# Optimization experiments

Measured on AMD Instinct MI355X. Metric: run time of the kernel, lower is better.

## Reference

```python
import jax, jax.numpy as jnp
import numpy as np

B, L, D = 2, 2048, 2048
NH, HD = 16, 128
SCALE = HD ** -0.5


def setup_inputs() -> dict:
    key = jax.random.key(0)
    ks = jax.random.split(key, 9)
    s = D ** -0.5  # roughly torch Linear init scale
    return {
        "hidden_states": jax.random.normal(ks[0], (B, L, D), dtype=jnp.float32),
        "Wq": jax.random.normal(ks[1], (NH * HD, D), dtype=jnp.float32) * s,
        "bq": jnp.zeros((NH * HD,), dtype=jnp.float32),
        "Wk": jax.random.normal(ks[2], (NH * HD, D), dtype=jnp.float32) * s,
        "bk": jnp.zeros((NH * HD,), dtype=jnp.float32),
        "Wv": jax.random.normal(ks[3], (NH * HD, D), dtype=jnp.float32) * s,
        "bv": jnp.zeros((NH * HD,), dtype=jnp.float32),
        "Wo": jax.random.normal(ks[4], (D, NH * HD), dtype=jnp.float32) * s,
        "bo": jnp.zeros((D,), dtype=jnp.float32),
    }


def reference(hidden_states, Wq, bq, Wk, bk, Wv, bv, Wo, bo):
    # projections (torch Linear: x @ W.T + b), split into heads: b s h d
    q = (hidden_states @ Wq.T + bq).reshape(B, L, NH, HD)
    k = (hidden_states @ Wk.T + bk).reshape(B, L, NH, HD)
    v = (hidden_states @ Wv.T + bv).reshape(B, L, NH, HD)
    # scores: [B, NH, L, L]
    scores = jnp.einsum("bqhd,bkhd->bhqk", q, k) * SCALE
    causal = jnp.tril(jnp.ones((L, L), dtype=bool))  # True = keep
    scores = jnp.where(causal, scores, jnp.float32(-jnp.inf))
    probs = jax.nn.softmax(scores, axis=-1)
    out = jnp.einsum("bhqk,bkhd->bqhd", probs, v).reshape(B, L, NH * HD)
    return out @ Wo.T + bo
```

## Files before the change

### kernel.cpp

```cpp
#include <hip/hip_runtime.h>

#define B_  2
#define L_  2048
#define D_  2048
#define NH_ 16
#define HD_ 128

typedef __bf16 bf16_t;
typedef __bf16 bf16x8 __attribute__((ext_vector_type(8)));
typedef __bf16 bf16x4 __attribute__((ext_vector_type(4)));
typedef float  f32x4  __attribute__((ext_vector_type(4)));

typedef const __attribute__((address_space(1))) void* gas_ptr;
typedef __attribute__((address_space(3))) void* las_ptr;

__device__ __forceinline__ void g2l16(const void* g, void* l) {
    __builtin_amdgcn_global_load_lds((gas_ptr)g, (las_ptr)l, 16, 0, 0);
}

__device__ __forceinline__ void raw_barrier() {
    asm volatile("s_barrier" ::: "memory");
}
__device__ __forceinline__ void wait_vm8() {
    asm volatile("s_waitcnt vmcnt(8)" ::: "memory");
}
__device__ __forceinline__ void wait_vm4() {
    asm volatile("s_waitcnt vmcnt(4)" ::: "memory");
}
__device__ __forceinline__ void wait_vm0() {
    asm volatile("s_waitcnt vmcnt(0)" ::: "memory");
}

__global__ __launch_bounds__(256) void cvt_all(const float* __restrict__ X,
                                               const float* __restrict__ Wq,
                                               const float* __restrict__ Wk,
                                               const float* __restrict__ Wv,
                                               const float* __restrict__ Wo,
                                               bf16_t* __restrict__ Xb,
                                               bf16_t* __restrict__ Wqkvb,
                                               bf16_t* __restrict__ Wob) {
    int i = blockIdx.x * 256 + threadIdx.x;
    const float* src;
    bf16_t* dst;
    int off;
    if (i < 2097152) { src = X; dst = Xb; off = i; }
    else {
        int j = i - 2097152;
        int w = j >> 20;
        off = j & 1048575;
        src = (w == 0) ? Wq : (w == 1) ? Wk : (w == 2) ? Wv : Wo;
        dst = (w == 3) ? Wob : Wqkvb + (size_t)w * 4194304;
    }
    float4 v = ((const float4*)src)[off];
    bf16x4 o;
    o[0] = (bf16_t)v.x; o[1] = (bf16_t)v.y; o[2] = (bf16_t)v.z; o[3] = (bf16_t)v.w;
    ((bf16x4*)dst)[off] = o;
}

__global__ __launch_bounds__(256) void gemm_bt(const bf16_t* __restrict__ A,
                                               const bf16_t* __restrict__ Bw,
                                               const float* __restrict__ bias,
                                               float* __restrict__ C,
                                               int M, int N, int K) {
    constexpr int BK = 32;
    __shared__ __align__(16) bf16_t smem[16384];
    const int tid  = threadIdx.x;
    const int wave = tid >> 6, lane = tid & 63;
    const int quad = lane >> 4, l16 = lane & 15;
    const int tm = blockIdx.y * 128, tn = blockIdx.x * 128;
    const int wm = (wave >> 1) * 64, wn = (wave & 1) * 64;

    const int srow = wave * 16 + (lane >> 2);
    const int scol = (lane & 3) * 8;
    const bf16_t* Ag = A  + (size_t)(tm + srow) * K + scol;
    const bf16_t* Bg = Bw + (size_t)(tn + srow) * K + scol;
    const size_t rowskip = (size_t)64 * K;

    auto stage = [&](int k0, int p) {
        bf16_t* a = smem + p * 4096 + (wave * 16) * BK;
        bf16_t* bl = smem + 8192 + p * 4096 + (wave * 16) * BK;
        g2l16(Ag + k0, a);
        g2l16(Ag + k0 + rowskip, a + 64 * BK);
        g2l16(Bg + k0, bl);
        g2l16(Bg + k0 + rowskip, bl + 64 * BK);
    };

    f32x4 acc[4][4] = {};
    const int niter = K / BK;
    stage(0, 0);

    for (int i = 0; i < niter; ++i) {
        const int p = i & 1;
        if (i + 1 < niter) { stage((i + 1) * BK, p ^ 1); wait_vm4(); }
        else wait_vm0();
        raw_barrier();

        const bf16_t* Alp = smem + p * 4096;
        const bf16_t* Blp = smem + 8192 + p * 4096;
        bf16x8 af[4], bf[4];
#pragma unroll
        for (int ii = 0; ii < 4; ++ii)
            af[ii] = *(const bf16x8*)(Alp + (wm + ii * 16 + l16) * BK + quad * 8);
#pragma unroll
        for (int j = 0; j < 4; ++j)
            bf[j] = *(const bf16x8*)(Blp + (wn + j * 16 + l16) * BK + quad * 8);
#pragma unroll
        for (int ii = 0; ii < 4; ++ii)
#pragma unroll
            for (int j = 0; j < 4; ++j)
                acc[ii][j] = __builtin_amdgcn_mfma_f32_16x16x32_bf16(af[ii], bf[j], acc[ii][j], 0, 0, 0);
        raw_barrier();
    }

#pragma unroll
    for (int j = 0; j < 4; ++j) {
        const int col = tn + wn + j * 16 + l16;
        const float bv = bias[col];
#pragma unroll
        for (int i = 0; i < 4; ++i) {
            const int row0 = tm + wm + i * 16 + quad * 4;
#pragma unroll
            for (int r = 0; r < 4; ++r)
                C[(size_t)(row0 + r) * N + col] = acc[i][j][r] + bv;
        }
    }
}

__global__ __launch_bounds__(256) void gemm_qkv(const bf16_t* __restrict__ A,
                                                const bf16_t* __restrict__ Bw,
                                                const float* __restrict__ b0,
                                                const float* __restrict__ b1,
                                                const float* __restrict__ b2,
                                                bf16_t* __restrict__ QK,
                                                bf16_t* __restrict__ Vt) {
    constexpr int BK = 32, K = D_;
    __shared__ __align__(16) bf16_t smem[17408];
    const int tid  = threadIdx.x;
    const int wave = tid >> 6, lane = tid & 63;
    const int quad = lane >> 4, l16 = lane & 15;
    const int tm = blockIdx.y * 128, tn = blockIdx.x * 128;
    const int wm = (wave >> 1) * 64, wn = (wave & 1) * 64;

    const int seg = tn >> 11;
    const float* bias = (seg == 0) ? b0 : (seg == 1) ? b1 : b2;

    const int srow = wave * 16 + (lane >> 2);
    const int scol = (lane & 3) * 8;
    const bf16_t* Ag = A  + (size_t)(tm + srow) * K + scol;
    const bf16_t* Bg = Bw + (size_t)(tn + srow) * K + scol;
    const size_t rowskip = (size_t)64 * K;

    auto stage = [&](int k0, int p) {
        bf16_t* a = smem + p * 4096 + (wave * 16) * BK;
        bf16_t* bl = smem + 8192 + p * 4096 + (wave * 16) * BK;
        g2l16(Ag + k0, a);
        g2l16(Ag + k0 + rowskip, a + 64 * BK);
        g2l16(Bg + k0, bl);
        g2l16(Bg + k0 + rowskip, bl + 64 * BK);
    };

    f32x4 acc[4][4] = {};
    const int niter = K / BK;
    stage(0, 0);

    for (int i = 0; i < niter; ++i) {
        const int p = i & 1;
        if (i + 1 < niter) { stage((i + 1) * BK, p ^ 1); wait_vm4(); }
        else wait_vm0();
        raw_barrier();

        const bf16_t* Alp = smem + p * 4096;
        const bf16_t* Blp = smem + 8192 + p * 4096;
        bf16x8 af[4], bf[4];
#pragma unroll
        for (int ii = 0; ii < 4; ++ii)
            af[ii] = *(const bf16x8*)(Alp + (wm + ii * 16 + l16) * BK + quad * 8);
#pragma unroll
        for (int j = 0; j < 4; ++j)
            bf[j] = *(const bf16x8*)(Blp + (wn + j * 16 + l16) * BK + quad * 8);
#pragma unroll
        for (int ii = 0; ii < 4; ++ii)
#pragma unroll
            for (int j = 0; j < 4; ++j)
                acc[ii][j] = __builtin_amdgcn_mfma_f32_16x16x32_bf16(af[ii], bf[j], acc[ii][j], 0, 0, 0);
        raw_barrier();
    }

    if (seg < 2) {
#pragma unroll
        for (int j = 0; j < 4; ++j) {
            const int col = tn + wn + j * 16 + l16;
            const float bv = bias[col & 2047];
#pragma unroll
            for (int i = 0; i < 4; ++i) {
                const int row0 = tm + wm + i * 16 + quad * 4;
#pragma unroll
                for (int r = 0; r < 4; ++r)
                    QK[(size_t)(row0 + r) * 4096 + col] = (bf16_t)(acc[i][j][r] + bv);
            }
        }
    } else {
        const int h = (tn >> 7) - 32;
        const int b = tm >> 11;
        const int tokbase = tm & 2047;
        __syncthreads();
#pragma unroll
        for (int j = 0; j < 4; ++j) {
            const int d = wn + j * 16 + l16;
            const float bv = bias[(tn + wn + j * 16 + l16) & 2047];
#pragma unroll
            for (int i = 0; i < 4; ++i)
#pragma unroll
                for (int r = 0; r < 4; ++r) {
                    const int tok = wm + i * 16 + quad * 4 + r;
                    smem[d * 136 + (((tok >> 3) ^ (d & 7)) << 3) + (tok & 7)] =
                        (bf16_t)(acc[i][j][r] + bv);
                }
        }
        __syncthreads();
        const int d = tid >> 1, half = tid & 1;
        bf16_t* gp = Vt + ((size_t)(b * NH_ + h) * HD_ + d) * L_ + tokbase + half * 64;
#pragma unroll
        for (int c2 = 0; c2 < 8; ++c2) {
            const int cc = half * 8 + c2;
            bf16x8 v = *(const bf16x8*)(smem + d * 136 + ((cc ^ (d & 7)) << 3));
            *(bf16x8*)(gp + c2 * 8) = v;
        }
    }
}

__global__ __launch_bounds__(256, 2) void attn_kernel(const bf16_t* __restrict__ QK,
                                                      const bf16_t* __restrict__ Vt,
                                                      bf16_t* __restrict__ Ctx) {
    constexpr float SCALE = 0.08838834764831845f;
    constexpr float MFIX  = 8.0f;
    const int bid = blockIdx.x;
    const int bh = bid & 31;
    const int qt = 15 - (bid >> 5);
    const int b = bh >> 4, h = bh & 15;
    const int tid = threadIdx.x, wave = tid >> 6, lane = tid & 63;
    const int quad = lane >> 4, l16 = lane & 15;
    const int q0 = qt * 128;

    __shared__ bf16_t Kl[2][64 * 128];
    __shared__ bf16_t Vl[2][128 * 64];
    __shared__ bf16_t Pl[4][16 * 72];

    bf16x8 qf[2][4];
#pragma unroll
    for (int s = 0; s < 2; ++s) {
        const bf16_t* qp = QK + (size_t)(b * L_ + q0 + wave * 32 + s * 16 + l16) * 4096 + h * HD_ + quad * 8;
#pragma unroll
        for (int ks = 0; ks < 4; ++ks) qf[s][ks] = *(const bf16x8*)(qp + ks * 32);
    }

    bf16x8 ones;
#pragma unroll
    for (int j = 0; j < 8; ++j) ones[j] = (bf16_t)1.0f;

    f32x4 oacc[2][8] = {};
    f32x4 lacc[2] = {};

    const bf16_t* Kg = QK + (size_t)(b * L_) * 4096 + 2048 + h * HD_;
    const bf16_t* Vg = Vt + (size_t)(bh * HD_) * L_;

    auto stage = [&](int tile, int p) {
        const bf16_t* kg = Kg + (size_t)tile * 64 * 4096;
        const bf16_t* vg = Vg + tile * 64;
#pragma unroll
        for (int c = 0; c < 4; ++c) {
            int row = c * 16 + wave * 4 + (lane >> 4);
            int gcol = ((lane & 15) ^ (row & 15)) * 8;
            g2l16(kg + (size_t)row * 4096 + gcol, &Kl[p][(c * 16 + wave * 4) * 128]);
        }
#pragma unroll
        for (int c = 0; c < 4; ++c) {
            int row = c * 32 + wave * 8 + (lane >> 3);
            int gcol = ((lane & 7) ^ (row & 7)) * 8;
            g2l16(vg + (size_t)row * L_ + gcol, &Vl[p][(c * 32 + wave * 8) * 64]);
        }
    };

    const int n = 2 * qt + 2;
    stage(0, 0);

    for (int it = 0; it < n; ++it) {
        const int p = it & 1;
        if (it + 1 < n) {
            stage(it + 1, p ^ 1);
            wait_vm8();
        } else {
            wait_vm0();
        }
        raw_barrier();

        const int kb = it * 64;
        const bool need_mask = (it >= n - 2);

        f32x4 sa[2][4] = {};
#pragma unroll
        for (int nt = 0; nt < 4; ++nt) {
            const int krow = nt * 16 + l16;
#pragma unroll
            for (int ks = 0; ks < 4; ++ks) {
                bf16x8 kf = *(const bf16x8*)(&Kl[p][krow * 128 + (((ks * 4 + quad) ^ l16) * 8)]);
                sa[0][nt] = __builtin_amdgcn_mfma_f32_16x16x32_bf16(qf[0][ks], kf, sa[0][nt], 0, 0, 0);
                sa[1][nt] = __builtin_amdgcn_mfma_f32_16x16x32_bf16(qf[1][ks], kf, sa[1][nt], 0, 0, 0);
            }
        }

        bf16x8 pf0[2], pf1[2];
#pragma unroll
        for (int nt = 0; nt < 4; ++nt)
#pragma unroll
            for (int r = 0; r < 4; ++r) {
                float sv = sa[0][nt][r] * SCALE - MFIX;
                if (need_mask) {
                    const int key = kb + nt * 16 + l16;
                    const int qq = q0 + wave * 32 + quad * 4 + r;
                    sv = (key <= qq) ? sv : -1e30f;
                }
                Pl[wave][(quad * 4 + r) * 72 + nt * 16 + l16] = (bf16_t)__expf(sv);
            }
        pf0[0] = *(const bf16x8*)(&Pl[wave][l16 * 72 + quad * 8]);
        pf0[1] = *(const bf16x8*)(&Pl[wave][l16 * 72 + 32 + quad * 8]);

#pragma unroll
        for (int nt = 0; nt < 4; ++nt)
#pragma unroll
            for (int r = 0; r < 4; ++r) {
                float sv = sa[1][nt][r] * SCALE - MFIX;
                if (need_mask) {
                    const int key = kb + nt * 16 + l16;
                    const int qq = q0 + wave * 32 + 16 + quad * 4 + r;
                    sv = (key <= qq) ? sv : -1e30f;
                }
                Pl[wave][(quad * 4 + r) * 72 + nt * 16 + l16] = (bf16_t)__expf(sv);
            }
        pf1[0] = *(const bf16x8*)(&Pl[wave][l16 * 72 + quad * 8]);
        pf1[1] = *(const bf16x8*)(&Pl[wave][l16 * 72 + 32 + quad * 8]);

        lacc[0] = __builtin_amdgcn_mfma_f32_16x16x32_bf16(pf0[0], ones, lacc[0], 0, 0, 0);
        lacc[0] = __builtin_amdgcn_mfma_f32_16x16x32_bf16(pf0[1], ones, lacc[0], 0, 0, 0);
        lacc[1] = __builtin_amdgcn_mfma_f32_16x16x32_bf16(pf1[0], ones, lacc[1], 0, 0, 0);
        lacc[1] = __builtin_amdgcn_mfma_f32_16x16x32_bf16(pf1[1], ones, lacc[1], 0, 0, 0);

#pragma unroll
        for (int dt = 0; dt < 8; ++dt) {
            const int drow = dt * 16 + l16;
#pragma unroll
            for (int ks = 0; ks < 2; ++ks) {
                bf16x8 vf = *(const bf16x8*)(&Vl[p][drow * 64 + (((ks * 4 + quad) ^ (drow & 7)) * 8)]);
                oacc[0][dt] = __builtin_amdgcn_mfma_f32_16x16x32_bf16(pf0[ks], vf, oacc[0][dt], 0, 0, 0);
                oacc[1][dt] = __builtin_amdgcn_mfma_f32_16x16x32_bf16(pf1[ks], vf, oacc[1][dt], 0, 0, 0);
            }
        }
        raw_barrier();
    }

#pragma unroll
    for (int s = 0; s < 2; ++s)
#pragma unroll
        for (int r = 0; r < 4; ++r) {
            const float inv = 1.0f / lacc[s][r];
            const int q = q0 + wave * 32 + s * 16 + quad * 4 + r;
            bf16_t* cp = Ctx + (size_t)(b * L_ + q) * 2048 + h * HD_;
#pragma unroll
            for (int dt = 0; dt < 8; ++dt)
                cp[dt * 16 + l16] = (bf16_t)(oacc[s][dt][r] * inv);
        }
}

extern "C" void kernel_launch(void* const* d_in, const int* in_sizes, int n_in,
                              void* d_out, int out_size, void* d_ws, size_t ws_size,
                              hipStream_t stream) {
    const float* X  = (const float*)d_in[0];
    const float* Wq = (const float*)d_in[1];
    const float* bq = (const float*)d_in[2];
    const float* Wk = (const float*)d_in[3];
    const float* bk = (const float*)d_in[4];
    const float* Wv = (const float*)d_in[5];
    const float* bv = (const float*)d_in[6];
    const float* Wo = (const float*)d_in[7];
    const float* bo = (const float*)d_in[8];
    float* out = (float*)d_out;

    char* ws = (char*)d_ws;
    bf16_t* Xb   = (bf16_t*)(ws);
    bf16_t* Ctx  = (bf16_t*)(ws);
    bf16_t* Wqkv = (bf16_t*)(ws + 16777216);
    bf16_t* Wob  = (bf16_t*)(ws + 41943040);
    bf16_t* QKb  = (bf16_t*)(ws + 50331648);
    bf16_t* Vtb  = (bf16_t*)(ws + 83886080);

    cvt_all<<<24576, 256, 0, stream>>>(X, Wq, Wk, Wv, Wo, Xb, Wqkv, Wob);

    gemm_qkv<<<dim3(48, 32), 256, 0, stream>>>(Xb, Wqkv, bq, bk, bv, QKb, Vtb);

    attn_kernel<<<dim3(512), 256, 0, stream>>>(QKb, Vtb, Ctx);

    gemm_bt<<<dim3(16, 32), 256, 0, stream>>>(Ctx, Wob, bo, out,
                                              B_ * L_, D_, D_);
}
```

Before: 380.7 us.

## Rewrite QKV GEMM with 256x256 tiles, 8 waves, swizzled LDS and interleaved staging

Rewrites the fused QKV projection GEMM to use 256x256 output tiles with 512 threads, BK=64 and XOR-swizzled LDS layout. Global-to-LDS loads for the next K tile are split into quarters and interleaved between four MFMA sub-phases, with s_setprio raised around the MFMA bursts. The V transpose epilogue now goes through per-wave LDS regions. This aims to raise arithmetic intensity and cut LDS bank conflicts, at the cost of more registers, 128KB LDS per block and a grid of only 384 blocks.

```diff
diff --git a/kernel.cpp b/kernel.cpp
--- a/kernel.cpp
+++ b/kernel.cpp
@@ -26,6 +26,9 @@
 }
 __device__ __forceinline__ void wait_vm4() {
     asm volatile("s_waitcnt vmcnt(4)" ::: "memory");
+}
+__device__ __forceinline__ void wait_vm2() {
+    asm volatile("s_waitcnt vmcnt(2)" ::: "memory");
 }
 __device__ __forceinline__ void wait_vm0() {
     asm volatile("s_waitcnt vmcnt(0)" ::: "memory");
@@ -126,105 +129,185 @@
     }
 }
 
-__global__ __launch_bounds__(256) void gemm_qkv(const bf16_t* __restrict__ A,
-                                                const bf16_t* __restrict__ Bw,
-                                                const float* __restrict__ b0,
-                                                const float* __restrict__ b1,
-                                                const float* __restrict__ b2,
-                                                bf16_t* __restrict__ QK,
-                                                bf16_t* __restrict__ Vt) {
-    constexpr int BK = 32, K = D_;
-    __shared__ __align__(16) bf16_t smem[17408];
+__global__ __launch_bounds__(512, 2) void gemm_qkv(const bf16_t* __restrict__ A,
+                                                   const bf16_t* __restrict__ Bw,
+                                                   const float* __restrict__ b0,
+                                                   const float* __restrict__ b1,
+                                                   const float* __restrict__ b2,
+                                                   bf16_t* __restrict__ QK,
+                                                   bf16_t* __restrict__ Vt) {
+    constexpr int K  = D_;
+    constexpr int BK = 64;
+    constexpr int NT = K / BK;
+    __shared__ __align__(16) bf16_t smem[65536];
+
     const int tid  = threadIdx.x;
     const int wave = tid >> 6, lane = tid & 63;
     const int quad = lane >> 4, l16 = lane & 15;
-    const int tm = blockIdx.y * 128, tn = blockIdx.x * 128;
-    const int wm = (wave >> 1) * 64, wn = (wave & 1) * 64;
-
+    const int tm = blockIdx.y * 256, tn = blockIdx.x * 256;
+    const int wm = (wave >> 2) * 128;
+    const int wn = (wave & 3) * 64;
     const int seg = tn >> 11;
-    const float* bias = (seg == 0) ? b0 : (seg == 1) ? b1 : b2;
-
-    const int srow = wave * 16 + (lane >> 2);
-    const int scol = (lane & 3) * 8;
-    const bf16_t* Ag = A  + (size_t)(tm + srow) * K + scol;
-    const bf16_t* Bg = Bw + (size_t)(tn + srow) * K + scol;
-    const size_t rowskip = (size_t)64 * K;
-
-    auto stage = [&](int k0, int p) {
-        bf16_t* a = smem + p * 4096 + (wave * 16) * BK;
-        bf16_t* bl = smem + 8192 + p * 4096 + (wave * 16) * BK;
-        g2l16(Ag + k0, a);
-        g2l16(Ag + k0 + rowskip, a + 64 * BK);
-        g2l16(Bg + k0, bl);
-        g2l16(Bg + k0 + rowskip, bl + 64 * BK);
+
+    const int srow = tid >> 3;
+    const int sg   = (tid & 7) ^ (srow & 7);
+    const bf16_t* Ag = A  + (size_t)(tm + srow) * K + sg * 8;
+    const bf16_t* Bg = Bw + (size_t)(tn + srow) * K + sg * 8;
+    const int ldsw = wave * 512;
+
+    auto stageA = [&](int t, int h) {
+        bf16_t* l = smem + (t & 1) * 32768 + h * 8192 + ldsw;
+        const bf16_t* g = Ag + (size_t)h * 128 * K + t * BK;
+        g2l16(g, l);
+        g2l16(g + (size_t)64 * K, l + 4096);
     };
-
-    f32x4 acc[4][4] = {};
-    const int niter = K / BK;
-    stage(0, 0);
-
-    for (int i = 0; i < niter; ++i) {
-        const int p = i & 1;
-        if (i + 1 < niter) { stage((i + 1) * BK, p ^ 1); wait_vm4(); }
-        else wait_vm0();
-        raw_barrier();
-
-        const bf16_t* Alp = smem + p * 4096;
-        const bf16_t* Blp = smem + 8192 + p * 4096;
-        bf16x8 af[4], bf[4];
-#pragma unroll
-        for (int ii = 0; ii < 4; ++ii)
-            af[ii] = *(const bf16x8*)(Alp + (wm + ii * 16 + l16) * BK + quad * 8);
-#pragma unroll
-        for (int j = 0; j < 4; ++j)
-            bf[j] = *(const bf16x8*)(Blp + (wn + j * 16 + l16) * BK + quad * 8);
-#pragma unroll
-        for (int ii = 0; ii < 4; ++ii)
-#pragma unroll
-            for (int j = 0; j < 4; ++j)
-                acc[ii][j] = __builtin_amdgcn_mfma_f32_16x16x32_bf16(af[ii], bf[j], acc[ii][j], 0, 0, 0);
-        raw_barrier();
+    auto stageB = [&](int t, int h) {
+        bf16_t* l = smem + (t & 1) * 32768 + 16384 + h * 8192 + ldsw;
+        const bf16_t* g = Bg + (size_t)h * 128 * K + t * BK;
+        g2l16(g, l);
+        g2l16(g + (size_t)64 * K, l + 4096);
+    };
+
+    f32x4 acc[8][4] = {};
+
+    stageA(0, 0); stageA(0, 1); stageB(0, 0); stageB(0, 1);
+
+    const int abase_w = (wave >> 2) * 8192;
+    const int bbase_w = 16384 + ((wave >> 1) & 1) * 8192;
+    const int brow0   = (wave & 1) * 64;
+
+    for (int t = 0; t < NT; ++t) {
+        const int p = t & 1;
+        const bf16_t* Ah = smem + p * 32768 + abase_w;
+        const bf16_t* Bh = smem + p * 32768 + bbase_w;
+        bf16x8 af[4][2], bfr[2][2];
+
+        raw_barrier();
+        if (t + 1 < NT) { stageA(t + 1, 0); wait_vm2(); } else wait_vm0();
+        raw_barrier();
+#pragma unroll
+        for (int mb = 0; mb < 4; ++mb)
+#pragma unroll
+            for (int ks = 0; ks < 2; ++ks) {
+                const int row = mb * 16 + l16;
+                af[mb][ks] = *(const bf16x8*)(Ah + row * 64 + (((ks * 4 + quad) ^ (row & 7)) << 3));
+            }
+#pragma unroll
+        for (int nb = 0; nb < 2; ++nb)
+#pragma unroll
+            for (int ks = 0; ks < 2; ++ks) {
+                const int row = brow0 + nb * 16 + l16;
+                bfr[nb][ks] = *(const bf16x8*)(Bh + row * 64 + (((ks * 4 + quad) ^ (row & 7)) << 3));
+            }
+        __builtin_amdgcn_s_setprio(1);
+#pragma unroll
+        for (int mb = 0; mb < 4; ++mb)
+#pragma unroll
+            for (int nb = 0; nb < 2; ++nb)
+#pragma unroll
+                for (int ks = 0; ks < 2; ++ks)
+                    acc[mb][nb] = __builtin_amdgcn_mfma_f32_16x16x32_bf16(af[mb][ks], bfr[nb][ks], acc[mb][nb], 0, 0, 0);
+        __builtin_amdgcn_s_setprio(0);
+
+        if (t + 1 < NT) stageA(t + 1, 1);
+        raw_barrier();
+#pragma unroll
+        for (int nb = 0; nb < 2; ++nb)
+#pragma unroll
+            for (int ks = 0; ks < 2; ++ks) {
+                const int row = brow0 + (nb + 2) * 16 + l16;
+                bfr[nb][ks] = *(const bf16x8*)(Bh + row * 64 + (((ks * 4 + quad) ^ (row & 7)) << 3));
+            }
+        __builtin_amdgcn_s_setprio(1);
+#pragma unroll
+        for (int mb = 0; mb < 4; ++mb)
+#pragma unroll
+            for (int nb = 0; nb < 2; ++nb)
+#pragma unroll
+                for (int ks = 0; ks < 2; ++ks)
+                    acc[mb][nb + 2] = __builtin_amdgcn_mfma_f32_16x16x32_bf16(af[mb][ks], bfr[nb][ks], acc[mb][nb + 2], 0, 0, 0);
+        __builtin_amdgcn_s_setprio(0);
+
+        if (t + 1 < NT) stageB(t + 1, 0);
+        raw_barrier();
+#pragma unroll
+        for (int mb = 0; mb < 4; ++mb)
+#pragma unroll
+            for (int ks = 0; ks < 2; ++ks) {
+                const int row = (mb + 4) * 16 + l16;
+                af[mb][ks] = *(const bf16x8*)(Ah + row * 64 + (((ks * 4 + quad) ^ (row & 7)) << 3));
+            }
+        __builtin_amdgcn_s_setprio(1);
+#pragma unroll
+        for (int mb = 0; mb < 4; ++mb)
+#pragma unroll
+            for (int nb = 0; nb < 2; ++nb)
+#pragma unroll
+                for (int ks = 0; ks < 2; ++ks)
+                    acc[mb + 4][nb + 2] = __builtin_amdgcn_mfma_f32_16x16x32_bf16(af[mb][ks], bfr[nb][ks], acc[mb + 4][nb + 2], 0, 0, 0);
+        __builtin_amdgcn_s_setprio(0);
+
+        if (t + 1 < NT) stageB(t + 1, 1);
+        raw_barrier();
+#pragma unroll
+        for (int nb = 0; nb < 2; ++nb)
+#pragma unroll
+            for (int ks = 0; ks < 2; ++ks) {
+                const int row = brow0 + nb * 16 + l16;
+                bfr[nb][ks] = *(const bf16x8*)(Bh + row * 64 + (((ks * 4 + quad) ^ (row & 7)) << 3));
+            }
+        __builtin_amdgcn_s_setprio(1);
+#pragma unroll
+        for (int mb = 0; mb < 4; ++mb)
+#pragma unroll
+            for (int nb = 0; nb < 2; ++nb)
+#pragma unroll
+                for (int ks = 0; ks < 2; ++ks)
+                    acc[mb + 4][nb] = __builtin_amdgcn_mfma_f32_16x16x32_bf16(af[mb][ks], bfr[nb][ks], acc[mb + 4][nb], 0, 0, 0);
+        __builtin_amdgcn_s_setprio(0);
     }
 
     if (seg < 2) {
-#pragma unroll
-        for (int j = 0; j < 4; ++j) {
-            const int col = tn + wn + j * 16 + l16;
+        const float* bias = (seg == 0) ? b0 : b1;
+#pragma unroll
+        for (int nb = 0; nb < 4; ++nb) {
+            const int col = tn + wn + nb * 16 + l16;
             const float bv = bias[col & 2047];
 #pragma unroll
-            for (int i = 0; i < 4; ++i) {
-                const int row0 = tm + wm + i * 16 + quad * 4;
+            for (int mb = 0; mb < 8; ++mb) {
+                const int row0 = tm + wm + mb * 16 + quad * 4;
 #pragma unroll
                 for (int r = 0; r < 4; ++r)
-                    QK[(size_t)(row0 + r) * 4096 + col] = (bf16_t)(acc[i][j][r] + bv);
+                    QK[(size_t)(row0 + r) * 4096 + col] = (bf16_t)(acc[mb][nb][r] + bv);
             }
         }
     } else {
-        const int h = (tn >> 7) - 32;
-        const int b = tm >> 11;
-        const int tokbase = tm & 2047;
         __syncthreads();
-#pragma unroll
-        for (int j = 0; j < 4; ++j) {
-            const int d = wn + j * 16 + l16;
-            const float bv = bias[(tn + wn + j * 16 + l16) & 2047];
-#pragma unroll
-            for (int i = 0; i < 4; ++i)
+        bf16_t* Tw = smem + wave * 8192;
+        const int colbase = (tn - 4096) + wn;
+#pragma unroll
+        for (int nb = 0; nb < 4; ++nb) {
+            const int d = nb * 16 + l16;
+            const float bv = b2[colbase + d];
+#pragma unroll
+            for (int mb = 0; mb < 8; ++mb)
 #pragma unroll
                 for (int r = 0; r < 4; ++r) {
-                    const int tok = wm + i * 16 + quad * 4 + r;
-                    smem[d * 136 + (((tok >> 3) ^ (d & 7)) << 3) + (tok & 7)] =
-                        (bf16_t)(acc[i][j][r] + bv);
+                    const int tok = mb * 16 + quad * 4 + r;
+                    Tw[d * 128 + ((((tok >> 3) ^ (d & 7)) << 3) | (tok & 7))] =
+                        (bf16_t)(acc[mb][nb][r] + bv);
                 }
         }
-        __syncthreads();
-        const int d = tid >> 1, half = tid & 1;
-        bf16_t* gp = Vt + ((size_t)(b * NH_ + h) * HD_ + d) * L_ + tokbase + half * 64;
-#pragma unroll
-        for (int c2 = 0; c2 < 8; ++c2) {
-            const int cc = half * 8 + c2;
-            bf16x8 v = *(const bf16x8*)(smem + d * 136 + ((cc ^ (d & 7)) << 3));
-            *(bf16x8*)(gp + c2 * 8) = v;
+        const int dl = lane;
+        const int h  = (colbase + dl) >> 7;
+        const int dg = (colbase + dl) & 127;
+        const int b  = tm >> 11;
+        const int tokbase = (tm & 2047) + wm;
+        bf16_t* gp = Vt + ((size_t)(b * NH_ + h) * HD_ + dg) * L_ + tokbase;
+#pragma unroll
+        for (int c = 0; c < 16; ++c) {
+            bf16x8 v = *(const bf16x8*)(Tw + dl * 128 + ((c ^ (dl & 7)) << 3));
+            *(bf16x8*)(gp + c * 8) = v;
         }
     }
 }
@@ -395,7 +478,7 @@
 
     cvt_all<<<24576, 256, 0, stream>>>(X, Wq, Wk, Wv, Wo, Xb, Wqkv, Wob);
 
-    gemm_qkv<<<dim3(48, 32), 256, 0, stream>>>(Xb, Wqkv, bq, bk, bv, QKb, Vtb);
+    gemm_qkv<<<dim3(24, 16), 512, 0, stream>>>(Xb, Wqkv, bq, bk, bv, QKb, Vtb);
 
     attn_kernel<<<dim3(512), 256, 0, stream>>>(QKb, Vtb, Ctx);
 
```

New measurement: 365.2 us. 4.1% less time.
